# Performance work log

Hardware: AMD Instinct MI355X
Metric: run time of the kernel (lower is better)

Reference implementation:

```python
import jax, jax.numpy as jnp
import numpy as np

T_KD = 20.0      # KL_divergence temperature
T_THR = 6.0      # Threshold_weights temperature
EPS = 1e-05


def _margin(o, gathered):
    # torch.sort descending, take top-2; margin only when target is the argmax value
    top2 = jax.lax.top_k(o, 2)[0]                      # [B, 2]
    return jnp.where(top2[:, 0] == gathered, top2[:, 0] - top2[:, 1], 0.0)


def _forward(outputs1, outputs2, outputs3, outputs4, out_s, targets):
    B = targets.shape[0]
    idx = jnp.arange(B)
    mimic = (outputs1 + outputs2 + outputs3 + outputs4) / 4.0

    teachers = [outputs1, outputs2, outputs3, outputs4, mimic]
    gathered = [t[idx, targets] for t in teachers]      # each [B]

    # C = min over gathered target logits of the 4 real teachers
    C = jnp.minimum(jnp.minimum(gathered[0].min(), gathered[1].min()),
                    jnp.minimum(gathered[2].min(), gathered[3].min()))
    # if C < 0: shift everything by (-C + eps); else no shift
    shift = jnp.where(C < 0, -C + EPS, 0.0)

    shifted = [t + shift for t in teachers]
    g_shift = [g + shift for g in gathered]

    # Threshold_weights: margin per branch, softmax over 5 branches
    preds = jnp.stack([_margin(s, g) for s, g in zip(shifted, g_shift)], axis=1)  # [B,5]
    out_threshold = jax.nn.softmax(preds / T_THR, axis=1)

    # max over the 4 (shifted) teacher logit tensors
    max_preds = jnp.maximum(jnp.maximum(shifted[0].max(), shifted[1].max()),
                            jnp.maximum(shifted[2].max(), shifted[3].max()))

    # per-sample CE of student (shared across branches)
    log_p_s = jax.nn.log_softmax(out_s, axis=1)
    CE = -log_p_s[idx, targets]                          # [B]

    log_ps_T = jax.nn.log_softmax(out_s / T_KD, axis=1)  # [B,C]

    def branch_loss(teacher, g_s):
        w2 = g_s / max_preds          # weights2
        w1 = 1.0 - w2                 # weights1
        log_pt = jax.nn.log_softmax(teacher / T_KD, axis=1)
        p_t = jnp.exp(log_pt)
        KD = jnp.sum(p_t * (log_pt - log_ps_T), axis=1) * (T_KD * T_KD)  # [B]
        return w1 * CE + w2 * KD

    # KD/CE use the ORIGINAL (unshifted) teacher logits
    losses = jnp.stack([branch_loss(t, g) for t, g in zip(teachers, g_shift)], axis=1)  # [B,5]
    return jnp.mean(jnp.sum(out_threshold * losses, axis=1))


def setup_inputs() -> dict:
    key = jax.random.key(0)
    ks = jax.random.split(key, 6)
    B, C = 8192, 1000
    return {
        "outputs1": jax.random.normal(ks[0], (B, C), dtype=jnp.float32),
        "outputs2": jax.random.normal(ks[1], (B, C), dtype=jnp.float32),
        "outputs3": jax.random.normal(ks[2], (B, C), dtype=jnp.float32),
        "outputs4": jax.random.normal(ks[3], (B, C), dtype=jnp.float32),
        "out_s": jax.random.normal(ks[4], (B, C), dtype=jnp.float32),
        "targets": jax.random.randint(ks[5], (B,), 0, C, dtype=jnp.int64 if jax.config.jax_enable_x64 else jnp.int32),
    }


def reference(outputs1, outputs2, outputs3, outputs4, out_s, targets):
    return _forward(outputs1, outputs2, outputs3, outputs4, out_s, targets)
```

## Files before the change

### kernel.cpp

```cpp
#include <hip/hip_runtime.h>
#include <math.h>

#define NB 8192
#define NC 1000
#define NF4 250


#define LOG2E 1.4426950408889634f
#define LN2   0.6931471805599453f

__device__ __forceinline__ float fexp2(float x) { return __builtin_amdgcn_exp2f(x); }
__device__ __forceinline__ float flog2(float x) { return __builtin_amdgcn_logf(x); }

template <int CTRL>
__device__ __forceinline__ float dpp_mov(float v, float ident) {
  return __uint_as_float((unsigned)__builtin_amdgcn_update_dpp(
      (int)__float_as_uint(ident), (int)__float_as_uint(v), CTRL, 0xF, 0xF,
      false));
}

__device__ __forceinline__ float dppredsum(float v) {
  v += dpp_mov<0x111>(v, 0.f);
  v += dpp_mov<0x112>(v, 0.f);
  v += dpp_mov<0x114>(v, 0.f);
  v += dpp_mov<0x118>(v, 0.f);
  v += dpp_mov<0x142>(v, 0.f);
  v += dpp_mov<0x143>(v, 0.f);
  return v;
}

__device__ __forceinline__ void dppredtop2(float& t1, float& t2) {
  const float NI = -INFINITY;
#define T2STEP(C)                                   \
  {                                                 \
    float i1 = dpp_mov<C>(t1, NI);                  \
    float i2 = dpp_mov<C>(t2, NI);                  \
    t2 = fmaxf(fmaxf(t2, i2), fminf(t1, i1));       \
    t1 = fmaxf(t1, i1);                             \
  }
  T2STEP(0x111) T2STEP(0x112) T2STEP(0x114) T2STEP(0x118)
  T2STEP(0x142) T2STEP(0x143)
#undef T2STEP
}

__device__ __forceinline__ float wredsum(float v) {
#pragma unroll
  for (int m = 32; m >= 1; m >>= 1) v += __shfl_xor(v, m, 64);
  return v;
}
__device__ __forceinline__ float wredmax(float v) {
#pragma unroll
  for (int m = 32; m >= 1; m >>= 1) v = fmaxf(v, __shfl_xor(v, m, 64));
  return v;
}
__device__ __forceinline__ float wredmin(float v) {
#pragma unroll
  for (int m = 32; m >= 1; m >>= 1) v = fminf(v, __shfl_xor(v, m, 64));
  return v;
}
__device__ __forceinline__ float f4get(const float4& v, int e) {
  return e == 0 ? v.x : e == 1 ? v.y : e == 2 ? v.z : v.w;
}

__global__ __launch_bounds__(256) void k_rowstats(
    const float* __restrict__ o1, const float* __restrict__ o2,
    const float* __restrict__ o3, const float* __restrict__ o4,
    const float* __restrict__ os, const int* __restrict__ tg,
    float* __restrict__ ws) {
  const int lane = threadIdx.x & 63;
  const int wv = threadIdx.x >> 6;
  const int row = blockIdx.x;
  const size_t base = (size_t)row * NC;
  const int f = (threadIdx.x < NF4) ? (int)threadIdx.x : 0;
  const bool act = threadIdx.x < NF4;

  float g1 = 0.f, g2 = 0.f, g3 = 0.f, g4 = 0.f, gs = 0.f;
  if (wv == 0) {
    const int target = tg[row];
    g1 = o1[base + target];
    g2 = o2[base + target];
    g3 = o3[base + target];
    g4 = o4[base + target];
    gs = os[base + target];
  }

  const float4 c1 = ((const float4*)(o1 + base))[f];
  const float4 c2 = ((const float4*)(o2 + base))[f];
  const float4 c3 = ((const float4*)(o3 + base))[f];
  const float4 c4 = ((const float4*)(o4 + base))[f];
  const float4 cs = ((const float4*)(os + base))[f];

  float t1[5], t2[5], Z[5], S1[5];
#pragma unroll
  for (int t = 0; t < 5; ++t) {
    t1[t] = -INFINITY; t2[t] = -INFINITY; Z[t] = 0.f; S1[t] = 0.f;
  }
  float Z1 = 0.f, Z20 = 0.f;
  const float K20 = LOG2E / 20.0f;

  if (act) {
#pragma unroll
    for (int e = 0; e < 4; ++e) {
      float w0 = f4get(c1, e);
      float w1 = f4get(c2, e);
      float w2 = f4get(c3, e);
      float w3 = f4get(c4, e);
      float wsv = f4get(cs, e);
      float wm = ((w0 + w1) + w2 + w3) * 0.25f;
      float w[5] = {w0, w1, w2, w3, wm};
#pragma unroll
      for (int t = 0; t < 5; ++t) {
        t2[t] = fmaxf(t2[t], fminf(t1[t], w[t]));
        t1[t] = fmaxf(t1[t], w[t]);
        float et = fexp2(w[t] * K20);
        Z[t] += et;
        S1[t] = fmaf(et, w[t] - wsv, S1[t]);
      }
      Z1 += fexp2(wsv * LOG2E);
      Z20 += fexp2(wsv * K20);
    }
  }

#pragma unroll
  for (int t = 0; t < 5; ++t) dppredtop2(t1[t], t2[t]);
#pragma unroll
  for (int t = 0; t < 5; ++t) { Z[t] = dppredsum(Z[t]); S1[t] = dppredsum(S1[t]); }
  Z1 = dppredsum(Z1);
  Z20 = dppredsum(Z20);

  __shared__ float sred[4][22];
  if (lane == 63) {
#pragma unroll
    for (int t = 0; t < 5; ++t) {
      sred[wv][t] = t1[t];
      sred[wv][5 + t] = t2[t];
      sred[wv][10 + t] = Z[t];
      sred[wv][15 + t] = S1[t];
    }
    sred[wv][20] = Z1;
    sred[wv][21] = Z20;
  }
  __syncthreads();

  if (threadIdx.x == 0) {
    float T1[5], T2[5], ZZ[5], SS[5], z1, z20;
#pragma unroll
    for (int t = 0; t < 5; ++t) {
      T1[t] = sred[0][t]; T2[t] = sred[0][5 + t];
      ZZ[t] = sred[0][10 + t]; SS[t] = sred[0][15 + t];
    }
    z1 = sred[0][20]; z20 = sred[0][21];
#pragma unroll
    for (int w = 1; w < 4; ++w) {
#pragma unroll
      for (int t = 0; t < 5; ++t) {
        float a1 = sred[w][t], a2 = sred[w][5 + t];
        float lo = fminf(T1[t], a1);
        T1[t] = fmaxf(T1[t], a1);
        T2[t] = fmaxf(fmaxf(T2[t], a2), lo);
        ZZ[t] += sred[w][10 + t];
        SS[t] += sred[w][15 + t];
      }
      z1 += sred[w][20];
      z20 += sred[w][21];
    }

    const float gm = ((g1 + g2) + g3 + g4) * 0.25f;
    float gg[5] = {g1, g2, g3, g4, gm};

    const float lse_s = flog2(z20) * LN2;
    const float CE = flog2(z1) * LN2 - gs;

#pragma unroll
    for (int t = 0; t < 5; ++t) {
      float lse_t = flog2(ZZ[t]) * LN2;
      float KD = 400.0f * (SS[t] / (20.0f * ZZ[t]) - lse_t + lse_s);
      float margin = (T1[t] == gg[t]) ? (T1[t] - T2[t]) : 0.0f;
      ws[(size_t)t * NB + row] = margin;
      ws[(size_t)(5 + t) * NB + row] = gg[t];
      ws[(size_t)(10 + t) * NB + row] = KD;
    }
    ws[(size_t)15 * NB + row] = CE;
    ws[(size_t)16 * NB + row] = fminf(fminf(g1, g2), fminf(g3, g4));
    ws[(size_t)17 * NB + row] = fmaxf(fmaxf(T1[0], T1[1]), fmaxf(T1[2], T1[3]));
  }
}

__global__ __launch_bounds__(1024) void k_minmax(float* __restrict__ ws,
                                                 float* __restrict__ out) {
  const int tid = threadIdx.x;
  const int lane = tid & 63, wv = tid >> 6;
  __shared__ float sA[16], sB[16];

  float mn = INFINITY, mx = -INFINITY;
  for (int r = tid; r < NB; r += 1024) {
    mn = fminf(mn, ws[(size_t)16 * NB + r]);
    mx = fmaxf(mx, ws[(size_t)17 * NB + r]);
  }
  mn = wredmin(mn);
  mx = wredmax(mx);
  if (lane == 0) { sA[wv] = mn; sB[wv] = mx; }
  __syncthreads();
  if (tid == 0) {
    float a = sA[0], b = sB[0];
    for (int i = 1; i < 16; ++i) { a = fminf(a, sA[i]); b = fmaxf(b, sB[i]); }
    float shift = (a < 0.0f) ? (-a + 1e-5f) : 0.0f;
    ws[(size_t)18 * NB] = shift;
    ws[(size_t)18 * NB + 1] = b + shift;
    out[0] = 0.0f;
  }
}

__global__ __launch_bounds__(256) void k_loss(const float* __restrict__ ws,
                                              float* __restrict__ out) {
  const int tid = threadIdx.x;
  const int lane = tid & 63, wv = tid >> 6;
  const int r = blockIdx.x * 256 + tid;
  __shared__ float sA[4];

  const float shift = ws[(size_t)18 * NB];
  const float maxp = ws[(size_t)18 * NB + 1];
  const float K6 = LOG2E / 6.0f;

  float m[5], e[5];
#pragma unroll
  for (int t = 0; t < 5; ++t) m[t] = ws[(size_t)t * NB + r];
  float pm = fmaxf(fmaxf(fmaxf(m[0], m[1]), fmaxf(m[2], m[3])), m[4]);
  float Zl = 0.0f;
#pragma unroll
  for (int t = 0; t < 5; ++t) { e[t] = fexp2((m[t] - pm) * K6); Zl += e[t]; }
  float ce = ws[(size_t)15 * NB + r];
  float rl = 0.0f;
#pragma unroll
  for (int t = 0; t < 5; ++t) {
    float g = ws[(size_t)(5 + t) * NB + r];
    float kd = ws[(size_t)(10 + t) * NB + r];
    float w2 = (g + shift) / maxp;
    float loss = (1.0f - w2) * ce + w2 * kd;
    rl += e[t] * loss;
  }
  float acc = rl / Zl;

  acc = wredsum(acc);
  if (lane == 0) sA[wv] = acc;
  __syncthreads();
  if (tid == 0) {
    float tot = (sA[0] + sA[1]) + (sA[2] + sA[3]);
    atomicAdd(out, tot * (1.0f / 8192.0f));
  }
}

extern "C" void kernel_launch(void* const* d_in, const int* in_sizes, int n_in,
                              void* d_out, int out_size, void* d_ws, size_t ws_size,
                              hipStream_t stream) {
  const float* o1 = (const float*)d_in[0];
  const float* o2 = (const float*)d_in[1];
  const float* o3 = (const float*)d_in[2];
  const float* o4 = (const float*)d_in[3];
  const float* os = (const float*)d_in[4];
  const int* tg = (const int*)d_in[5];
  float* ws = (float*)d_ws;
  float* out = (float*)d_out;

  k_rowstats<<<NB, 256, 0, stream>>>(o1, o2, o3, o4, os, tg, ws);
  k_minmax<<<1, 1024, 0, stream>>>(ws, out);
  k_loss<<<NB / 256, 256, 0, stream>>>(ws, out);
}
```

Before: 188.2 us.

## Process eight rows per block with register prefetch of the next row

The row-statistics kernel now handles eight rows per block instead of one and launches an eighth as many blocks. While the current row is reduced, the block loads the next row's five float4 slices and target logits into registers, aiming to hide global load latency behind compute. In exchange it adds a second __syncthreads per row, uses more registers, and exposes less block-level parallelism.

```diff
diff --git a/kernel.cpp b/kernel.cpp
--- a/kernel.cpp
+++ b/kernel.cpp
@@ -4,6 +4,7 @@
 #define NB 8192
 #define NC 1000
 #define NF4 250
+#define RPB 8
 
 
 #define LOG2E 1.4426950408889634f
@@ -67,122 +68,156 @@
     const float* __restrict__ o3, const float* __restrict__ o4,
     const float* __restrict__ os, const int* __restrict__ tg,
     float* __restrict__ ws) {
-  const int lane = threadIdx.x & 63;
-  const int wv = threadIdx.x >> 6;
-  const int row = blockIdx.x;
-  const size_t base = (size_t)row * NC;
-  const int f = (threadIdx.x < NF4) ? (int)threadIdx.x : 0;
-  const bool act = threadIdx.x < NF4;
-
+  const int tid = threadIdx.x;
+  const int lane = tid & 63;
+  const int wv = tid >> 6;
+  const int row0 = blockIdx.x * RPB;
+  const int f = (tid < NF4) ? tid : 0;
+  const bool act = tid < NF4;
+  const float K20 = LOG2E / 20.0f;
+
+  int tgt[RPB];
+#pragma unroll
+  for (int i = 0; i < RPB; ++i) tgt[i] = tg[row0 + i];
+
+  size_t base = (size_t)row0 * NC;
+  float4 c1 = ((const float4*)(o1 + base))[f];
+  float4 c2 = ((const float4*)(o2 + base))[f];
+  float4 c3 = ((const float4*)(o3 + base))[f];
+  float4 c4 = ((const float4*)(o4 + base))[f];
+  float4 cs = ((const float4*)(os + base))[f];
   float g1 = 0.f, g2 = 0.f, g3 = 0.f, g4 = 0.f, gs = 0.f;
   if (wv == 0) {
-    const int target = tg[row];
-    g1 = o1[base + target];
-    g2 = o2[base + target];
-    g3 = o3[base + target];
-    g4 = o4[base + target];
-    gs = os[base + target];
-  }
-
-  const float4 c1 = ((const float4*)(o1 + base))[f];
-  const float4 c2 = ((const float4*)(o2 + base))[f];
-  const float4 c3 = ((const float4*)(o3 + base))[f];
-  const float4 c4 = ((const float4*)(o4 + base))[f];
-  const float4 cs = ((const float4*)(os + base))[f];
-
-  float t1[5], t2[5], Z[5], S1[5];
-#pragma unroll
-  for (int t = 0; t < 5; ++t) {
-    t1[t] = -INFINITY; t2[t] = -INFINITY; Z[t] = 0.f; S1[t] = 0.f;
-  }
-  float Z1 = 0.f, Z20 = 0.f;
-  const float K20 = LOG2E / 20.0f;
-
-  if (act) {
-#pragma unroll
-    for (int e = 0; e < 4; ++e) {
-      float w0 = f4get(c1, e);
-      float w1 = f4get(c2, e);
-      float w2 = f4get(c3, e);
-      float w3 = f4get(c4, e);
-      float wsv = f4get(cs, e);
-      float wm = ((w0 + w1) + w2 + w3) * 0.25f;
-      float w[5] = {w0, w1, w2, w3, wm};
+    g1 = o1[base + tgt[0]];
+    g2 = o2[base + tgt[0]];
+    g3 = o3[base + tgt[0]];
+    g4 = o4[base + tgt[0]];
+    gs = os[base + tgt[0]];
+  }
+
+  __shared__ float sred[4][22];
+
+#pragma unroll 1
+  for (int i = 0; i < RPB; ++i) {
+    const int row = row0 + i;
+
+    float4 n1, n2, n3, n4, n5;
+    float ng1 = 0.f, ng2 = 0.f, ng3 = 0.f, ng4 = 0.f, ng5 = 0.f;
+    const bool pf = (i + 1 < RPB);
+    if (pf) {
+      const size_t nb_ = (size_t)(row + 1) * NC;
+      n1 = ((const float4*)(o1 + nb_))[f];
+      n2 = ((const float4*)(o2 + nb_))[f];
+      n3 = ((const float4*)(o3 + nb_))[f];
+      n4 = ((const float4*)(o4 + nb_))[f];
+      n5 = ((const float4*)(os + nb_))[f];
+      if (wv == 0) {
+        ng1 = o1[nb_ + tgt[i + 1]];
+        ng2 = o2[nb_ + tgt[i + 1]];
+        ng3 = o3[nb_ + tgt[i + 1]];
+        ng4 = o4[nb_ + tgt[i + 1]];
+        ng5 = os[nb_ + tgt[i + 1]];
+      }
+    }
+
+    float t1[5], t2[5], Z[5], S1[5];
+#pragma unroll
+    for (int t = 0; t < 5; ++t) {
+      t1[t] = -INFINITY; t2[t] = -INFINITY; Z[t] = 0.f; S1[t] = 0.f;
+    }
+    float Z1 = 0.f, Z20 = 0.f;
+
+    if (act) {
+#pragma unroll
+      for (int e = 0; e < 4; ++e) {
+        float w0 = f4get(c1, e);
+        float w1 = f4get(c2, e);
+        float w2 = f4get(c3, e);
+        float w3 = f4get(c4, e);
+        float wsv = f4get(cs, e);
+        float wm = ((w0 + w1) + w2 + w3) * 0.25f;
+        float w[5] = {w0, w1, w2, w3, wm};
+#pragma unroll
+        for (int t = 0; t < 5; ++t) {
+          t2[t] = fmaxf(t2[t], fminf(t1[t], w[t]));
+          t1[t] = fmaxf(t1[t], w[t]);
+          float et = fexp2(w[t] * K20);
+          Z[t] += et;
+          S1[t] = fmaf(et, w[t] - wsv, S1[t]);
+        }
+        Z1 += fexp2(wsv * LOG2E);
+        Z20 += fexp2(wsv * K20);
+      }
+    }
+
+#pragma unroll
+    for (int t = 0; t < 5; ++t) dppredtop2(t1[t], t2[t]);
+#pragma unroll
+    for (int t = 0; t < 5; ++t) { Z[t] = dppredsum(Z[t]); S1[t] = dppredsum(S1[t]); }
+    Z1 = dppredsum(Z1);
+    Z20 = dppredsum(Z20);
+
+    if (lane == 63) {
 #pragma unroll
       for (int t = 0; t < 5; ++t) {
-        t2[t] = fmaxf(t2[t], fminf(t1[t], w[t]));
-        t1[t] = fmaxf(t1[t], w[t]);
-        float et = fexp2(w[t] * K20);
-        Z[t] += et;
-        S1[t] = fmaf(et, w[t] - wsv, S1[t]);
-      }
-      Z1 += fexp2(wsv * LOG2E);
-      Z20 += fexp2(wsv * K20);
-    }
-  }
-
-#pragma unroll
-  for (int t = 0; t < 5; ++t) dppredtop2(t1[t], t2[t]);
-#pragma unroll
-  for (int t = 0; t < 5; ++t) { Z[t] = dppredsum(Z[t]); S1[t] = dppredsum(S1[t]); }
-  Z1 = dppredsum(Z1);
-  Z20 = dppredsum(Z20);
-
-  __shared__ float sred[4][22];
-  if (lane == 63) {
-#pragma unroll
-    for (int t = 0; t < 5; ++t) {
-      sred[wv][t] = t1[t];
-      sred[wv][5 + t] = t2[t];
-      sred[wv][10 + t] = Z[t];
-      sred[wv][15 + t] = S1[t];
-    }
-    sred[wv][20] = Z1;
-    sred[wv][21] = Z20;
-  }
-  __syncthreads();
-
-  if (threadIdx.x == 0) {
-    float T1[5], T2[5], ZZ[5], SS[5], z1, z20;
-#pragma unroll
-    for (int t = 0; t < 5; ++t) {
-      T1[t] = sred[0][t]; T2[t] = sred[0][5 + t];
-      ZZ[t] = sred[0][10 + t]; SS[t] = sred[0][15 + t];
-    }
-    z1 = sred[0][20]; z20 = sred[0][21];
-#pragma unroll
-    for (int w = 1; w < 4; ++w) {
+        sred[wv][t] = t1[t];
+        sred[wv][5 + t] = t2[t];
+        sred[wv][10 + t] = Z[t];
+        sred[wv][15 + t] = S1[t];
+      }
+      sred[wv][20] = Z1;
+      sred[wv][21] = Z20;
+    }
+    __syncthreads();
+
+    if (tid == 0) {
+      float T1[5], T2[5], ZZ[5], SS[5], z1, z20;
 #pragma unroll
       for (int t = 0; t < 5; ++t) {
-        float a1 = sred[w][t], a2 = sred[w][5 + t];
-        float lo = fminf(T1[t], a1);
-        T1[t] = fmaxf(T1[t], a1);
-        T2[t] = fmaxf(fmaxf(T2[t], a2), lo);
-        ZZ[t] += sred[w][10 + t];
-        SS[t] += sred[w][15 + t];
-      }
-      z1 += sred[w][20];
-      z20 += sred[w][21];
-    }
-
-    const float gm = ((g1 + g2) + g3 + g4) * 0.25f;
-    float gg[5] = {g1, g2, g3, g4, gm};
-
-    const float lse_s = flog2(z20) * LN2;
-    const float CE = flog2(z1) * LN2 - gs;
-
-#pragma unroll
-    for (int t = 0; t < 5; ++t) {
-      float lse_t = flog2(ZZ[t]) * LN2;
-      float KD = 400.0f * (SS[t] / (20.0f * ZZ[t]) - lse_t + lse_s);
-      float margin = (T1[t] == gg[t]) ? (T1[t] - T2[t]) : 0.0f;
-      ws[(size_t)t * NB + row] = margin;
-      ws[(size_t)(5 + t) * NB + row] = gg[t];
-      ws[(size_t)(10 + t) * NB + row] = KD;
-    }
-    ws[(size_t)15 * NB + row] = CE;
-    ws[(size_t)16 * NB + row] = fminf(fminf(g1, g2), fminf(g3, g4));
-    ws[(size_t)17 * NB + row] = fmaxf(fmaxf(T1[0], T1[1]), fmaxf(T1[2], T1[3]));
+        T1[t] = sred[0][t]; T2[t] = sred[0][5 + t];
+        ZZ[t] = sred[0][10 + t]; SS[t] = sred[0][15 + t];
+      }
+      z1 = sred[0][20]; z20 = sred[0][21];
+#pragma unroll
+      for (int w = 1; w < 4; ++w) {
+#pragma unroll
+        for (int t = 0; t < 5; ++t) {
+          float a1 = sred[w][t], a2 = sred[w][5 + t];
+          float lo = fminf(T1[t], a1);
+          T1[t] = fmaxf(T1[t], a1);
+          T2[t] = fmaxf(fmaxf(T2[t], a2), lo);
+          ZZ[t] += sred[w][10 + t];
+          SS[t] += sred[w][15 + t];
+        }
+        z1 += sred[w][20];
+        z20 += sred[w][21];
+      }
+
+      const float gm = ((g1 + g2) + g3 + g4) * 0.25f;
+      float gg[5] = {g1, g2, g3, g4, gm};
+
+      const float lse_s = flog2(z20) * LN2;
+      const float CE = flog2(z1) * LN2 - gs;
+
+#pragma unroll
+      for (int t = 0; t < 5; ++t) {
+        float lse_t = flog2(ZZ[t]) * LN2;
+        float KD = 400.0f * (SS[t] / (20.0f * ZZ[t]) - lse_t + lse_s);
+        float margin = (T1[t] == gg[t]) ? (T1[t] - T2[t]) : 0.0f;
+        ws[(size_t)t * NB + row] = margin;
+        ws[(size_t)(5 + t) * NB + row] = gg[t];
+        ws[(size_t)(10 + t) * NB + row] = KD;
+      }
+      ws[(size_t)15 * NB + row] = CE;
+      ws[(size_t)16 * NB + row] = fminf(fminf(g1, g2), fminf(g3, g4));
+      ws[(size_t)17 * NB + row] = fmaxf(fmaxf(T1[0], T1[1]), fmaxf(T1[2], T1[3]));
+    }
+    __syncthreads();
+
+    if (pf) {
+      c1 = n1; c2 = n2; c3 = n3; c4 = n4; cs = n5;
+      g1 = ng1; g2 = ng2; g3 = ng3; g4 = ng4; gs = ng5;
+    }
   }
 }
 
@@ -262,7 +297,7 @@
   float* ws = (float*)d_ws;
   float* out = (float*)d_out;
 
-  k_rowstats<<<NB, 256, 0, stream>>>(o1, o2, o3, o4, os, tg, ws);
+  k_rowstats<<<NB / RPB, 256, 0, stream>>>(o1, o2, o3, o4, os, tg, ws);
   k_minmax<<<1, 1024, 0, stream>>>(ws, out);
   k_loss<<<NB / 256, 256, 0, stream>>>(ws, out);
 }
```

Measured after the change: 200.0 us. 1.06x slower.
